# Kernel optimization log

Hardware: AMD Instinct MI355X
Metric: run time of the kernel (lower is better)

Reference implementation:

```python
import jax, jax.numpy as jnp
import numpy as np

E = 1024
H = 16          # num_heads
D = E // H      # head_dim
HID = 1024      # hidden_dim
B, S = 16, 512
EPS = 1e-5


def _ln(x, g, b):
    mu = jnp.mean(x, axis=-1, keepdims=True)
    var = jnp.mean(jnp.square(x - mu), axis=-1, keepdims=True)
    return (x - mu) * jax.lax.rsqrt(var + EPS) * g + b


def setup_inputs() -> dict:
    key = jax.random.key(0)
    ks = jax.random.split(key, 8)
    s = 1.0 / np.sqrt(E)
    return {
        'state_features': jax.random.normal(ks[0], (6, B, S, E), jnp.float32),
        'Wq': jax.random.normal(ks[1], (E, E), jnp.float32) * s,
        'bq': jnp.zeros((E,), jnp.float32),
        'Wk': jax.random.normal(ks[2], (E, E), jnp.float32) * s,
        'bk': jnp.zeros((E,), jnp.float32),
        'Wv': jax.random.normal(ks[3], (E, E), jnp.float32) * s,
        'bv': jnp.zeros((E,), jnp.float32),
        'Wo': jax.random.normal(ks[4], (E, E), jnp.float32) * s,
        'bo': jnp.zeros((E,), jnp.float32),
        'ln1_g': jnp.ones((E,), jnp.float32),
        'ln1_b': jnp.zeros((E,), jnp.float32),
        'fusion_w': jnp.ones((6,), jnp.float32) / 6.0,
        'Wf': jax.random.normal(ks[5], (HID, E), jnp.float32) * s,
        'bf': jnp.zeros((HID,), jnp.float32),
        'ln2_g': jnp.ones((HID,), jnp.float32),
        'ln2_b': jnp.zeros((HID,), jnp.float32),
    }


def reference(state_features, Wq, bq, Wk, bk, Wv, bv, Wo, bo,
              ln1_g, ln1_b, fusion_w, Wf, bf, ln2_g, ln2_b):
    # state_features: (6, B, S, E) -> stacked (N, 6, E), N = B*S
    st = jnp.transpose(state_features, (1, 2, 0, 3)).reshape(B * S, 6, E)
    N = st.shape[0]

    q = (st @ Wq.T + bq).reshape(N, 6, H, D)
    k = (st @ Wk.T + bk).reshape(N, 6, H, D)
    v = (st @ Wv.T + bv).reshape(N, 6, H, D)

    # tiny 6x6 attention per token per head (dropout = identity in eval)
    scores = jnp.einsum('nqhd,nkhd->nhqk', q, k) / np.sqrt(D).astype(np.float32)
    attn = jax.nn.softmax(scores, axis=-1)
    ctx = jnp.einsum('nhqk,nkhd->nqhd', attn, v).reshape(N, 6, E)

    out = ctx @ Wo.T + bo
    enhanced = _ln(out + st, ln1_g, ln1_b)  # (N, 6, E)

    # weighted_sum fusion
    w = jax.nn.softmax(fusion_w)
    fused = jnp.einsum('nse,s->ne', enhanced, w)

    hidden = fused @ Wf.T + bf
    hidden = jnp.where(hidden >= 0, hidden, 0.01 * hidden)  # LeakyReLU(0.01)
    hidden = _ln(hidden, ln2_g, ln2_b)
    return hidden.reshape(B, S, HID)
```

## Files before the change

kernel.cpp:

```cpp
#include <hip/hip_runtime.h>
#include <hip/hip_bf16.h>

#define NTOK 8192
#define E 1024
#define NS 6
#define MBIG (NTOK * NS)
#define NSE ((long)NTOK * E)

typedef short short8 __attribute__((ext_vector_type(8)));
typedef float f32x4 __attribute__((ext_vector_type(4)));
typedef unsigned short ushort4v __attribute__((ext_vector_type(4)));

#define TM 128
#define TN 128
#define BK 64

static __device__ __forceinline__ float bf2f(unsigned short u) {
    union { unsigned int i; float f; } c; c.i = ((unsigned int)u) << 16; return c.f;
}

struct WPtrs { const float* s[5]; __hip_bfloat16* d[5]; };
__global__ __launch_bounds__(256) void cvt5_w(WPtrs p)
{
    const int seg = blockIdx.x >> 10;
    const int i = ((blockIdx.x & 1023) * 256 + threadIdx.x) * 4;
    const float4 v = *(const float4*)(p.s[seg] + i);
    union { __hip_bfloat16 h[4]; unsigned long long u; } pk;
    pk.h[0] = (__hip_bfloat16)v.x;
    pk.h[1] = (__hip_bfloat16)v.y;
    pk.h[2] = (__hip_bfloat16)v.z;
    pk.h[3] = (__hip_bfloat16)v.w;
    *(unsigned long long*)(p.d[seg] + i) = pk.u;
}

__global__ __launch_bounds__(256) void cvt_bulk(
    const float* __restrict__ src, __hip_bfloat16* __restrict__ dst)
{
    const long i = ((long)blockIdx.x * 256 + threadIdx.x) * 4;
    const float4 v = *(const float4*)(src + i);
    union { __hip_bfloat16 h[4]; unsigned long long u; } pk;
    pk.h[0] = (__hip_bfloat16)v.x;
    pk.h[1] = (__hip_bfloat16)v.y;
    pk.h[2] = (__hip_bfloat16)v.z;
    pk.h[3] = (__hip_bfloat16)v.w;
    *(unsigned long long*)(dst + i) = pk.u;
}

#define NITER  8

struct GOut { __hip_bfloat16* C[3]; const float* bias[3]; };

static __device__ __forceinline__ void stage_half(
    const __hip_bfloat16* gsrc,
    __hip_bfloat16* ldst, int tid)
{
#pragma unroll
    for (int piece = 0; piece < 2; ++piece) {
        const int r  = piece * 64 + (tid >> 3);
        const int s  = tid & 7;
        const int ss = s ^ (r & 7);
        const __hip_bfloat16* g = gsrc + (long)r * 1024 + ss * 8;
        __hip_bfloat16* l = ldst + r * 64 + s * 8;
        __builtin_amdgcn_global_load_lds((const __attribute__((address_space(1))) void*)g,
                                         (__attribute__((address_space(3))) void*)l, 16, 0, 0);
    }
}

static __device__ __forceinline__ short8 ld_frag(
    const __hip_bfloat16* half_base, int lr, int slot)
{
    return *(const short8*)(half_base + lr * 64 + ((slot ^ (lr & 7)) << 3));
}

#define STAGE(kt, part)                                                         \
  {                                                                             \
    const int _b  = (kt) & 1;                                                   \
    const int _ab = (part) >> 1;                                                \
    const int _hf = (part) & 1;                                                 \
    const __hip_bfloat16* _g = (_ab == 0)                                       \
        ? A  + (m0 + _hf * 128) * 1024 + (kt) * 64                              \
        : Wb + ((long)n0 + _hf * 128) * 1024 + (kt) * 64;                       \
    stage_half(_g, &lds[((_b * 2 + _ab) * 2 + _hf) * 8192], tid);               \
  }

#define PH(kt, q, HASNEXT, nkt, STMT_STAGE, STMT_WAIT)                          \
  {                                                                             \
    STMT_STAGE;                                                                 \
    STMT_WAIT;                                                                  \
    __builtin_amdgcn_s_barrier();                                               \
    asm volatile("s_waitcnt lgkmcnt(0)" ::: "memory");                          \
    __builtin_amdgcn_sched_barrier(0);                                          \
    __builtin_amdgcn_s_setprio(1);                                              \
    _Pragma("unroll") for (int mf = 0; mf < 2; ++mf)                            \
      _Pragma("unroll") for (int nf = 0; nf < 4; ++nf)                          \
        _Pragma("unroll") for (int k2 = 0; k2 < 2; ++k2)                        \
          acc[(q) * 2 + mf][nf] = __builtin_amdgcn_mfma_f32_16x16x32_bf16(      \
              bfr[nf][k2], afr[(q) & 1][mf][k2], acc[(q) * 2 + mf][nf], 0,0,0); \
    __builtin_amdgcn_s_setprio(0);                                              \
    if ((q) < 3) {                                                              \
      const __hip_bfloat16* _Ab = &lds[((((kt) & 1) * 2 + 0) * 2 + wm) * 8192]; \
      _Pragma("unroll") for (int mf = 0; mf < 2; ++mf)                          \
        _Pragma("unroll") for (int k2 = 0; k2 < 2; ++k2)                        \
          afr[((q) + 1) & 1][mf][k2] =                                          \
              ld_frag(_Ab, ((q) + 1) * 32 + mf * 16 + mrow, k2 * 4 + quad);     \
    } else if (HASNEXT) {                                                       \
      const __hip_bfloat16* _An = &lds[((((nkt) & 1) * 2 + 0) * 2 + wm) * 8192];\
      const __hip_bfloat16* _Bn =                                               \
          &lds[((((nkt) & 1) * 2 + 1) * 2 + (wn >> 1)) * 8192];                 \
      _Pragma("unroll") for (int nf = 0; nf < 4; ++nf)                          \
        _Pragma("unroll") for (int k2 = 0; k2 < 2; ++k2)                        \
          bfr[nf][k2] = ld_frag(_Bn, (wn & 1) * 64 + nf * 16 + mrow,            \
                                k2 * 4 + quad);                                 \
      _Pragma("unroll") for (int mf = 0; mf < 2; ++mf)                          \
        _Pragma("unroll") for (int k2 = 0; k2 < 2; ++k2)                        \
          afr[0][mf][k2] = ld_frag(_An, mf * 16 + mrow, k2 * 4 + quad);         \
    }                                                                           \
    __builtin_amdgcn_s_barrier();                                               \
  }

__global__ __launch_bounds__(512) void gemm256(
    const __hip_bfloat16* __restrict__ A,
    const __hip_bfloat16* __restrict__ Wb,
    GOut out)
{
    __shared__ __hip_bfloat16 lds[2 * 2 * 2 * 8192] __attribute__((aligned(16)));

    const int tid  = threadIdx.x;
    const int lane = tid & 63;
    const int wid  = tid >> 6;
    const int quad = lane >> 4;
    const int mrow = lane & 15;
    const int wm = wid >> 2;
    const int wn = wid & 3;

    const int gx  = gridDim.x;
    const int nwg = gx * gridDim.y;
    const int cpx = nwg >> 3;
    const int lin = blockIdx.y * gx + blockIdx.x;
    const int tile = (lin & 7) * cpx + (lin >> 3);
    const int  n0 = (tile % gx) * 256;
    const long m0 = (long)(tile / gx) * 256;

    f32x4 acc[8][4] = {};
    short8 bfr[4][2];
    short8 afr[2][2][2];

    STAGE(0, 0); STAGE(0, 1); STAGE(0, 2); STAGE(0, 3);
    STAGE(1, 2); STAGE(1, 3);
    asm volatile("s_waitcnt vmcnt(4)" ::: "memory");
    __builtin_amdgcn_s_barrier();

    {
        const __hip_bfloat16* _Ab = &lds[(0 * 2 + wm) * 8192];
        const __hip_bfloat16* _Bb = &lds[((0 * 2 + 1) * 2 + (wn >> 1)) * 8192];
#pragma unroll
        for (int nf = 0; nf < 4; ++nf)
#pragma unroll
            for (int k2 = 0; k2 < 2; ++k2)
                bfr[nf][k2] = ld_frag(_Bb, (wn & 1) * 64 + nf * 16 + mrow, k2 * 4 + quad);
#pragma unroll
        for (int mf = 0; mf < 2; ++mf)
#pragma unroll
            for (int k2 = 0; k2 < 2; ++k2)
                afr[0][mf][k2] = ld_frag(_Ab, mf * 16 + mrow, k2 * 4 + quad);
    }

#pragma unroll 1
    for (int it = 0; it < NITER; ++it) {
        const int kt0 = 2 * it;
        const int kt1 = 2 * it + 1;
        const bool more = (it < NITER - 1);

        PH(kt0, 0, true, kt0, STAGE(kt1, 0), ((void)0));
        PH(kt0, 1, true, kt0, STAGE(kt1, 1), ((void)0));
        PH(kt0, 2, true, kt0, if (more) STAGE(kt0 + 2, 2), ((void)0));
        PH(kt0, 3, true, kt1, if (more) STAGE(kt0 + 2, 3),
           if (more) { asm volatile("s_waitcnt vmcnt(4)" ::: "memory"); }
           else      { asm volatile("s_waitcnt vmcnt(0)" ::: "memory"); });
        PH(kt1, 0, true, kt1, if (more) STAGE(kt0 + 2, 0), ((void)0));
        PH(kt1, 1, true, kt1, if (more) STAGE(kt0 + 2, 1), ((void)0));
        PH(kt1, 2, true, kt1, if (more) STAGE(kt0 + 3, 2), ((void)0));
        PH(kt1, 3, more, kt0 + 2, if (more) STAGE(kt0 + 3, 3),
           if (more) { asm volatile("s_waitcnt vmcnt(4)" ::: "memory"); });
    }

    const int seg = n0 >> 10;
    const int nb  = n0 & 1023;
    __hip_bfloat16* Cp = out.C[seg];
    const float* bp = out.bias[seg];
#pragma unroll
    for (int mf = 0; mf < 8; ++mf) {
        const long row = m0 + wm * 128 + mf * 16 + mrow;
#pragma unroll
        for (int nf = 0; nf < 4; ++nf) {
            const int colb = nb + wn * 64 + nf * 16 + quad * 4;
            const f32x4 bv4 = *(const f32x4*)(bp + colb);
            union { __hip_bfloat16 h[4]; unsigned long long u; } pk;
#pragma unroll
            for (int r = 0; r < 4; ++r)
                pk.h[r] = (__hip_bfloat16)(acc[mf][nf][r] + bv4[r]);
            *(unsigned long long*)(Cp + row * 1024 + colb) = pk.u;
        }
    }
}

__global__ __launch_bounds__(256) void gemm_bt(
    const __hip_bfloat16* __restrict__ A,
    const __hip_bfloat16* __restrict__ Wb,
    const float* __restrict__ bias,
    __hip_bfloat16* __restrict__ C)
{
    __shared__ __hip_bfloat16 lA[TM * BK] __attribute__((aligned(16)));
    __shared__ __hip_bfloat16 lB[TN * BK] __attribute__((aligned(16)));

    const int tid  = threadIdx.x;
    const int wave = tid >> 6;
    const int lane = tid & 63;
    const int quad = lane >> 4;
    const int mrow = lane & 15;
    const int wr = wave >> 1;
    const int wc = wave & 1;

    const int Gy   = gridDim.y;
    const int lin  = blockIdx.y * 8 + blockIdx.x;
    const int tile = (lin & 7) * Gy + (lin >> 3);
    const int  n0 = (tile & 7) * TN;
    const long m0 = (long)(tile >> 3) * TM;

    const int srow = lane >> 3;
    const int scol = (lane & 7) * 8;

    f32x4 acc[4][4] = {};

    for (int k0 = 0; k0 < 1024; k0 += BK) {
        __syncthreads();
#pragma unroll
        for (int it = 0; it < 4; ++it) {
            const int chunk = it * 4 + wave;
            const int row   = chunk * 8 + srow;
            const __hip_bfloat16* ga = A + (m0 + row) * 1024 + k0 + scol;
            const __hip_bfloat16* gb = Wb + (long)(n0 + row) * 1024 + k0 + scol;
            __hip_bfloat16* la = lA + row * BK + scol;
            __hip_bfloat16* lb = lB + row * BK + scol;
            __builtin_amdgcn_global_load_lds((const __attribute__((address_space(1))) void*)ga,
                                             (__attribute__((address_space(3))) void*)la, 16, 0, 0);
            __builtin_amdgcn_global_load_lds((const __attribute__((address_space(1))) void*)gb,
                                             (__attribute__((address_space(3))) void*)lb, 16, 0, 0);
        }
        __syncthreads();

#pragma unroll
        for (int kk = 0; kk < BK; kk += 32) {
            short8 af[4], bfrg[4];
#pragma unroll
            for (int i = 0; i < 4; ++i)
                af[i] = *(const short8*)(lA + (wr * 64 + i * 16 + mrow) * BK + kk + quad * 8);
#pragma unroll
            for (int j = 0; j < 4; ++j)
                bfrg[j] = *(const short8*)(lB + (wc * 64 + j * 16 + mrow) * BK + kk + quad * 8);
#pragma unroll
            for (int i = 0; i < 4; ++i)
#pragma unroll
                for (int j = 0; j < 4; ++j)
                    acc[i][j] = __builtin_amdgcn_mfma_f32_16x16x32_bf16(af[i], bfrg[j], acc[i][j], 0, 0, 0);
        }
    }

#pragma unroll
    for (int i = 0; i < 4; ++i) {
#pragma unroll
        for (int j = 0; j < 4; ++j) {
            const int col = n0 + wc * 64 + j * 16 + mrow;
            const float bv = bias[col];
#pragma unroll
            for (int r = 0; r < 4; ++r) {
                const long row = m0 + wr * 64 + i * 16 + quad * 4 + r;
                C[row * 1024 + col] = (__hip_bfloat16)(acc[i][j][r] + bv);
            }
        }
    }
}

__global__ __launch_bounds__(256) void gemm_a32_bt(
    const float* __restrict__ A,
    const __hip_bfloat16* __restrict__ Wb,
    const float* __restrict__ bias,
    __hip_bfloat16* __restrict__ C)
{
    __shared__ __hip_bfloat16 lA[TM * BK] __attribute__((aligned(16)));
    __shared__ __hip_bfloat16 lB[TN * BK] __attribute__((aligned(16)));

    const int tid  = threadIdx.x;
    const int wave = tid >> 6;
    const int lane = tid & 63;
    const int quad = lane >> 4;
    const int mrow = lane & 15;
    const int wr = wave >> 1;
    const int wc = wave & 1;

    const int Gy   = gridDim.y;
    const int lin  = blockIdx.y * 8 + blockIdx.x;
    const int tile = (lin & 7) * Gy + (lin >> 3);
    const int  n0 = (tile & 7) * TN;
    const long m0 = (long)(tile >> 3) * TM;

    const int srow = lane >> 3;
    const int scol = (lane & 7) * 8;

    f32x4 acc[4][4] = {};

    for (int k0 = 0; k0 < 1024; k0 += BK) {
        __syncthreads();
#pragma unroll
        for (int it = 0; it < 4; ++it) {
            const int chunk = it * 4 + wave;
            const int row   = chunk * 8 + srow;
            const __hip_bfloat16* gb = Wb + (long)(n0 + row) * 1024 + k0 + scol;
            __hip_bfloat16* lb = lB + row * BK + scol;
            __builtin_amdgcn_global_load_lds((const __attribute__((address_space(1))) void*)gb,
                                             (__attribute__((address_space(3))) void*)lb, 16, 0, 0);
        }
#pragma unroll
        for (int u = 0; u < 8; ++u) {
            const int c   = u * 256 + tid;
            const int row = c >> 4;
            const int c4  = c & 15;
            const float4 av = *(const float4*)(A + (m0 + row) * 1024 + k0 + c4 * 4);
            union { __hip_bfloat16 h[4]; unsigned long long uu; } pk;
            pk.h[0] = (__hip_bfloat16)av.x;
            pk.h[1] = (__hip_bfloat16)av.y;
            pk.h[2] = (__hip_bfloat16)av.z;
            pk.h[3] = (__hip_bfloat16)av.w;
            *(unsigned long long*)(lA + row * BK + c4 * 4) = pk.uu;
        }
        __syncthreads();

#pragma unroll
        for (int kk = 0; kk < BK; kk += 32) {
            short8 af[4], bfrg[4];
#pragma unroll
            for (int i = 0; i < 4; ++i)
                af[i] = *(const short8*)(lA + (wr * 64 + i * 16 + mrow) * BK + kk + quad * 8);
#pragma unroll
            for (int j = 0; j < 4; ++j)
                bfrg[j] = *(const short8*)(lB + (wc * 64 + j * 16 + mrow) * BK + kk + quad * 8);
#pragma unroll
            for (int i = 0; i < 4; ++i)
#pragma unroll
                for (int j = 0; j < 4; ++j)
                    acc[i][j] = __builtin_amdgcn_mfma_f32_16x16x32_bf16(af[i], bfrg[j], acc[i][j], 0, 0, 0);
        }
    }

#pragma unroll
    for (int i = 0; i < 4; ++i) {
#pragma unroll
        for (int j = 0; j < 4; ++j) {
            const int col = n0 + wc * 64 + j * 16 + mrow;
            const float bv = bias[col];
#pragma unroll
            for (int r = 0; r < 4; ++r) {
                const long row = m0 + wr * 64 + i * 16 + quad * 4 + r;
                C[row * 1024 + col] = (__hip_bfloat16)(acc[i][j][r] + bv);
            }
        }
    }
}

__global__ __launch_bounds__(256) void attn6(
    const __hip_bfloat16* qb,
    const __hip_bfloat16* __restrict__ kb,
    const __hip_bfloat16* __restrict__ vb,
    __hip_bfloat16* ctx)
{
    const int w    = blockIdx.x * 4 + (threadIdx.x >> 6);
    const int lane = threadIdx.x & 63;
    const int n  = w >> 2;
    const int hg = w & 3;
    const int h  = hg * 4 + (lane >> 4);
    const int sub = lane & 15;
    const long base = (long)n * 1024 + h * 64 + sub * 4;

    float qf[NS][4], kf[NS][4], vf[NS][4];
#pragma unroll
    for (int s = 0; s < NS; ++s) {
        const ushort4v qs = *(const ushort4v*)(qb + s * NSE + base);
        const ushort4v ks = *(const ushort4v*)(kb + s * NSE + base);
        const ushort4v vs = *(const ushort4v*)(vb + s * NSE + base);
#pragma unroll
        for (int c = 0; c < 4; ++c) {
            qf[s][c] = bf2f(qs[c]);
            kf[s][c] = bf2f(ks[c]);
            vf[s][c] = bf2f(vs[c]);
        }
    }

    float p[NS][NS];
#pragma unroll
    for (int i = 0; i < NS; ++i)
#pragma unroll
        for (int j = 0; j < NS; ++j) {
            float t = qf[i][0] * kf[j][0];
            t = fmaf(qf[i][1], kf[j][1], t);
            t = fmaf(qf[i][2], kf[j][2], t);
            t = fmaf(qf[i][3], kf[j][3], t);
            t += __shfl_xor(t, 1, 64);
            t += __shfl_xor(t, 2, 64);
            t += __shfl_xor(t, 4, 64);
            t += __shfl_xor(t, 8, 64);
            p[i][j] = t * 0.125f;
        }

#pragma unroll
    for (int i = 0; i < NS; ++i) {
        float m = p[i][0];
#pragma unroll
        for (int j = 1; j < NS; ++j) m = fmaxf(m, p[i][j]);
        float sum = 0.f;
#pragma unroll
        for (int j = 0; j < NS; ++j) { p[i][j] = __expf(p[i][j] - m); sum += p[i][j]; }
        const float inv = 1.0f / sum;
        float a[4] = {0.f, 0.f, 0.f, 0.f};
#pragma unroll
        for (int j = 0; j < NS; ++j)
#pragma unroll
            for (int c = 0; c < 4; ++c) a[c] = fmaf(p[i][j], vf[j][c], a[c]);
        union { __hip_bfloat16 h4[4]; unsigned long long u; } pk;
#pragma unroll
        for (int c = 0; c < 4; ++c) pk.h4[c] = (__hip_bfloat16)(a[c] * inv);
        *(unsigned long long*)(ctx + i * NSE + base) = pk.u;
    }
}

__global__ __launch_bounds__(256) void ln1_fuse_bf(
    const __hip_bfloat16* __restrict__ wo_out,
    const __hip_bfloat16* __restrict__ sfb,
    const float* __restrict__ g,
    const float* __restrict__ b,
    const float* __restrict__ fw,
    __hip_bfloat16* __restrict__ fused)
{
    const int n = blockIdx.x, tid = threadIdx.x;
    const int wave = tid >> 6, lane = tid & 63;
    const int e0 = tid * 4;

    float w[NS];
    float mx = -1e30f;
#pragma unroll
    for (int s = 0; s < NS; ++s) { w[s] = fw[s]; mx = fmaxf(mx, w[s]); }
    float sw = 0.f;
#pragma unroll
    for (int s = 0; s < NS; ++s) { w[s] = __expf(w[s] - mx); sw += w[s]; }
    const float isw = 1.0f / sw;

    const f32x4 gv4 = *(const f32x4*)(g + e0);
    const f32x4 bv4 = *(const f32x4*)(b + e0);

    __shared__ float red[2][4];
    float accf[4] = {0.f, 0.f, 0.f, 0.f};

    for (int s = 0; s < NS; ++s) {
        const long base = s * NSE + (long)n * 1024 + e0;
        const ushort4v wv = *(const ushort4v*)(wo_out + base);
        const ushort4v sv = *(const ushort4v*)(sfb + base);
        float x[4];
        float sum = 0.f, sq = 0.f;
#pragma unroll
        for (int c = 0; c < 4; ++c) {
            x[c] = bf2f(wv[c]) + bf2f(sv[c]);
            sum += x[c];
            sq  += x[c] * x[c];
        }
#pragma unroll
        for (int off = 32; off; off >>= 1) {
            sum += __shfl_xor(sum, off, 64);
            sq  += __shfl_xor(sq,  off, 64);
        }
        if (lane == 0) { red[0][wave] = sum; red[1][wave] = sq; }
        __syncthreads();
        sum = red[0][0] + red[0][1] + red[0][2] + red[0][3];
        sq  = red[1][0] + red[1][1] + red[1][2] + red[1][3];
        __syncthreads();
        const float mu   = sum * (1.0f / 1024.0f);
        const float var  = sq * (1.0f / 1024.0f) - mu * mu;
        const float rstd = rsqrtf(var + 1e-5f);
        const float ws_  = w[s] * isw;
#pragma unroll
        for (int c = 0; c < 4; ++c)
            accf[c] += ws_ * ((x[c] - mu) * rstd * gv4[c] + bv4[c]);
    }
    union { __hip_bfloat16 h4[4]; unsigned long long u; } pk;
#pragma unroll
    for (int c = 0; c < 4; ++c) pk.h4[c] = (__hip_bfloat16)accf[c];
    *(unsigned long long*)(fused + (long)n * 1024 + e0) = pk.u;
}

__global__ __launch_bounds__(256) void ln1_fuse(
    const __hip_bfloat16* __restrict__ wo_out,
    const float* __restrict__ sf,
    const float* __restrict__ g,
    const float* __restrict__ b,
    const float* __restrict__ fw,
    __hip_bfloat16* __restrict__ fused)
{
    const int n = blockIdx.x, tid = threadIdx.x;
    const int wave = tid >> 6, lane = tid & 63;
    const int e0 = tid * 4;

    float w[NS];
    float mx = -1e30f;
#pragma unroll
    for (int s = 0; s < NS; ++s) { w[s] = fw[s]; mx = fmaxf(mx, w[s]); }
    float sw = 0.f;
#pragma unroll
    for (int s = 0; s < NS; ++s) { w[s] = __expf(w[s] - mx); sw += w[s]; }
    const float isw = 1.0f / sw;

    const f32x4 gv4 = *(const f32x4*)(g + e0);
    const f32x4 bv4 = *(const f32x4*)(b + e0);

    __shared__ float red[2][4];
    float accf[4] = {0.f, 0.f, 0.f, 0.f};

    for (int s = 0; s < NS; ++s) {
        const long base = s * NSE + (long)n * 1024 + e0;
        const ushort4v wv = *(const ushort4v*)(wo_out + base);
        const f32x4   sv = *(const f32x4*)(sf + base);
        float x[4];
        float sum = 0.f, sq = 0.f;
#pragma unroll
        for (int c = 0; c < 4; ++c) {
            x[c] = bf2f(wv[c]) + sv[c];
            sum += x[c];
            sq  += x[c] * x[c];
        }
#pragma unroll
        for (int off = 32; off; off >>= 1) {
            sum += __shfl_xor(sum, off, 64);
            sq  += __shfl_xor(sq,  off, 64);
        }
        if (lane == 0) { red[0][wave] = sum; red[1][wave] = sq; }
        __syncthreads();
        sum = red[0][0] + red[0][1] + red[0][2] + red[0][3];
        sq  = red[1][0] + red[1][1] + red[1][2] + red[1][3];
        __syncthreads();
        const float mu   = sum * (1.0f / 1024.0f);
        const float var  = sq * (1.0f / 1024.0f) - mu * mu;
        const float rstd = rsqrtf(var + 1e-5f);
        const float ws_  = w[s] * isw;
#pragma unroll
        for (int c = 0; c < 4; ++c)
            accf[c] += ws_ * ((x[c] - mu) * rstd * gv4[c] + bv4[c]);
    }
    union { __hip_bfloat16 h4[4]; unsigned long long u; } pk;
#pragma unroll
    for (int c = 0; c < 4; ++c) pk.h4[c] = (__hip_bfloat16)accf[c];
    *(unsigned long long*)(fused + (long)n * 1024 + e0) = pk.u;
}

__global__ __launch_bounds__(256) void ln2_out(
    const __hip_bfloat16* __restrict__ hidden,
    const float* __restrict__ g,
    const float* __restrict__ b,
    float* __restrict__ out)
{
    const int n = blockIdx.x, tid = threadIdx.x;
    const int wave = tid >> 6, lane = tid & 63;
    const int e0 = tid * 4;
    __shared__ float red[2][4];

    const ushort4v hv = *(const ushort4v*)(hidden + (long)n * 1024 + e0);
    float x[4];
    float sum = 0.f, sq = 0.f;
#pragma unroll
    for (int c = 0; c < 4; ++c) {
        float t = bf2f(hv[c]);
        t = t >= 0.f ? t : 0.01f * t;
        x[c] = t;
        sum += t;
        sq  += t * t;
    }
#pragma unroll
    for (int off = 32; off; off >>= 1) {
        sum += __shfl_xor(sum, off, 64);
        sq  += __shfl_xor(sq,  off, 64);
    }
    if (lane == 0) { red[0][wave] = sum; red[1][wave] = sq; }
    __syncthreads();
    sum = red[0][0] + red[0][1] + red[0][2] + red[0][3];
    sq  = red[1][0] + red[1][1] + red[1][2] + red[1][3];
    const float mu   = sum * (1.0f / 1024.0f);
    const float var  = sq * (1.0f / 1024.0f) - mu * mu;
    const float rstd = rsqrtf(var + 1e-5f);

    const f32x4 gv4 = *(const f32x4*)(g + e0);
    const f32x4 bv4 = *(const f32x4*)(b + e0);
    f32x4 o;
#pragma unroll
    for (int c = 0; c < 4; ++c)
        o[c] = (x[c] - mu) * rstd * gv4[c] + bv4[c];
    *(f32x4*)(out + (long)n * 1024 + e0) = o;
}

extern "C" void kernel_launch(void* const* d_in, const int* in_sizes, int n_in,
                              void* d_out, int out_size, void* d_ws, size_t ws_size,
                              hipStream_t stream)
{
    const float* SF  = (const float*)d_in[0];
    const float* Wq  = (const float*)d_in[1];
    const float* bq  = (const float*)d_in[2];
    const float* Wk  = (const float*)d_in[3];
    const float* bk  = (const float*)d_in[4];
    const float* Wv  = (const float*)d_in[5];
    const float* bv  = (const float*)d_in[6];
    const float* Wo  = (const float*)d_in[7];
    const float* bo  = (const float*)d_in[8];
    const float* g1  = (const float*)d_in[9];
    const float* b1  = (const float*)d_in[10];
    const float* fw  = (const float*)d_in[11];
    const float* Wf  = (const float*)d_in[12];
    const float* bf_ = (const float*)d_in[13];
    const float* g2  = (const float*)d_in[14];
    const float* b2  = (const float*)d_in[15];
    float* out = (float*)d_out;

    const size_t REG = (size_t)MBIG * 1024 * sizeof(__hip_bfloat16);
    const size_t WTS = (size_t)5 * 1024 * 1024 * sizeof(__hip_bfloat16);
    const bool big_ws = ws_size >= 4 * REG + WTS;

    __hip_bfloat16* r0  = (__hip_bfloat16*)d_ws;
    __hip_bfloat16* r1  = r0 + (long)MBIG * 1024;
    __hip_bfloat16* r2  = r1 + (long)MBIG * 1024;
    __hip_bfloat16* r3  = r2 + (long)MBIG * 1024;
    __hip_bfloat16* wb  = big_ws ? (r3 + (long)MBIG * 1024) : r3;
    __hip_bfloat16* Wqb = wb;
    __hip_bfloat16* Wkb = Wqb + 1024 * 1024;
    __hip_bfloat16* Wvb = Wkb + 1024 * 1024;
    __hip_bfloat16* Wob = Wvb + 1024 * 1024;
    __hip_bfloat16* Wfb = Wob + 1024 * 1024;

    const dim3 blk(256);

    WPtrs wp;
    wp.s[0] = Wq; wp.s[1] = Wk; wp.s[2] = Wv; wp.s[3] = Wo; wp.s[4] = Wf;
    wp.d[0] = Wqb; wp.d[1] = Wkb; wp.d[2] = Wvb; wp.d[3] = Wob; wp.d[4] = Wfb;
    cvt5_w<<<5 * 1024, blk, 0, stream>>>(wp);

    cvt_bulk<<<MBIG, blk, 0, stream>>>(SF, r2);

    if (big_ws) {
        const dim3 blk2(512);
        const dim3 gQKV(12, MBIG / 256);
        const dim3 gB2(4, MBIG / 256);

        GOut oqkv;
        oqkv.C[0] = r0; oqkv.C[1] = r1; oqkv.C[2] = r3;
        oqkv.bias[0] = bq; oqkv.bias[1] = bk; oqkv.bias[2] = bv;
        gemm256<<<gQKV, blk2, 0, stream>>>(r2, Wqb, oqkv);

        attn6<<<NTOK, blk, 0, stream>>>(r0, r1, r3, r0);

        GOut owo;
        owo.C[0] = r1; owo.C[1] = r1; owo.C[2] = r1;
        owo.bias[0] = bo; owo.bias[1] = bo; owo.bias[2] = bo;
        gemm256<<<gB2, blk2, 0, stream>>>(r0, Wob, owo);

        ln1_fuse_bf<<<NTOK, blk, 0, stream>>>(r1, r2, g1, b1, fw, r0);

        gemm_bt<<<dim3(8, NTOK / TM), blk, 0, stream>>>(r0, Wfb, bf_, r2);

        ln2_out<<<NTOK, blk, 0, stream>>>(r2, g2, b2, out);
    } else {
        const dim3 gBig(8, MBIG / TM);
        const dim3 gSm(8, NTOK / TM);

        gemm_bt<<<gBig, blk, 0, stream>>>(r2, Wqb, bq, r0);
        gemm_bt<<<gBig, blk, 0, stream>>>(r2, Wkb, bk, r1);
        gemm_a32_bt<<<gBig, blk, 0, stream>>>(SF, Wvb, bv, r2);
        attn6<<<NTOK, blk, 0, stream>>>(r0, r1, r2, r0);
        gemm_bt<<<gBig, blk, 0, stream>>>(r0, Wob, bo, r1);
        ln1_fuse<<<NTOK, blk, 0, stream>>>(r1, SF, g1, b1, fw, r2);
        gemm_bt<<<gSm, blk, 0, stream>>>(r2, Wfb, bf_, r0);
        ln2_out<<<NTOK, blk, 0, stream>>>(r0, g2, b2, out);
    }
}
```

Before: 921.4 us.

## Fuse residual add into Wo GEMM epilogue and use wave-per-row layernorm kernels

The Wo GEMM epilogue now adds the bf16 residual (converted state features) directly, so the layernorm-fusion kernel reads one bf16 tensor per slot instead of two. The LN1-fusion and LN2 kernels are rewritten so that one wavefront handles a whole 1024-wide row with 16 elements per lane. This removes the shared-memory reductions and block barriers in favour of pure wave shuffles. The residual is now rounded to bf16 together with the GEMM output before layernorm, which adds a little rounding error.

```diff
diff --git a/kernel.cpp b/kernel.cpp
--- a/kernel.cpp
+++ b/kernel.cpp
@@ -10,6 +10,7 @@
 typedef short short8 __attribute__((ext_vector_type(8)));
 typedef float f32x4 __attribute__((ext_vector_type(4)));
 typedef unsigned short ushort4v __attribute__((ext_vector_type(4)));
+typedef unsigned short ushort8v __attribute__((ext_vector_type(8)));
 
 #define TM 128
 #define TN 128
@@ -48,7 +49,7 @@
 
 #define NITER  8
 
-struct GOut { __hip_bfloat16* C[3]; const float* bias[3]; };
+struct GOut { __hip_bfloat16* C[3]; const float* bias[3]; const __hip_bfloat16* R; };
 
 static __device__ __forceinline__ void stage_half(
     const __hip_bfloat16* gsrc,
@@ -188,6 +189,7 @@
     const int nb  = n0 & 1023;
     __hip_bfloat16* Cp = out.C[seg];
     const float* bp = out.bias[seg];
+    const bool hasR = (out.R != nullptr);
 #pragma unroll
     for (int mf = 0; mf < 8; ++mf) {
         const long row = m0 + wm * 128 + mf * 16 + mrow;
@@ -195,10 +197,16 @@
         for (int nf = 0; nf < 4; ++nf) {
             const int colb = nb + wn * 64 + nf * 16 + quad * 4;
             const f32x4 bv4 = *(const f32x4*)(bp + colb);
+            float rs[4] = {0.f, 0.f, 0.f, 0.f};
+            if (hasR) {
+                const ushort4v rv = *(const ushort4v*)(out.R + row * 1024 + colb);
+#pragma unroll
+                for (int r = 0; r < 4; ++r) rs[r] = bf2f(rv[r]);
+            }
             union { __hip_bfloat16 h[4]; unsigned long long u; } pk;
 #pragma unroll
             for (int r = 0; r < 4; ++r)
-                pk.h[r] = (__hip_bfloat16)(acc[mf][nf][r] + bv4[r]);
+                pk.h[r] = (__hip_bfloat16)(acc[mf][nf][r] + bv4[r] + rs[r]);
             *(unsigned long long*)(Cp + row * 1024 + colb) = pk.u;
         }
     }
@@ -432,14 +440,80 @@
     }
 }
 
-__global__ __launch_bounds__(256) void ln1_fuse_bf(
-    const __hip_bfloat16* __restrict__ wo_out,
-    const __hip_bfloat16* __restrict__ sfb,
+__global__ __launch_bounds__(256) void ln1_fuse_w(
+    const __hip_bfloat16* __restrict__ enh,
     const float* __restrict__ g,
     const float* __restrict__ b,
     const float* __restrict__ fw,
     __hip_bfloat16* __restrict__ fused)
 {
+    const int wave = threadIdx.x >> 6, lane = threadIdx.x & 63;
+    const int n  = blockIdx.x * 4 + wave;
+    const int e0 = lane * 16;
+
+    float w[NS];
+    float mx = -1e30f;
+#pragma unroll
+    for (int s = 0; s < NS; ++s) { w[s] = fw[s]; mx = fmaxf(mx, w[s]); }
+    float sw = 0.f;
+#pragma unroll
+    for (int s = 0; s < NS; ++s) { w[s] = __expf(w[s] - mx); sw += w[s]; }
+    const float isw = 1.0f / sw;
+
+    f32x4 gq[4], bq4[4];
+#pragma unroll
+    for (int c4 = 0; c4 < 4; ++c4) {
+        gq[c4]  = *(const f32x4*)(g + e0 + c4 * 4);
+        bq4[c4] = *(const f32x4*)(b + e0 + c4 * 4);
+    }
+
+    float accf[16];
+#pragma unroll
+    for (int c = 0; c < 16; ++c) accf[c] = 0.f;
+
+#pragma unroll
+    for (int s = 0; s < NS; ++s) {
+        const long base = s * NSE + (long)n * 1024 + e0;
+        const ushort8v h0 = *(const ushort8v*)(enh + base);
+        const ushort8v h1 = *(const ushort8v*)(enh + base + 8);
+        float x[16];
+#pragma unroll
+        for (int c = 0; c < 8; ++c) { x[c] = bf2f(h0[c]); x[8 + c] = bf2f(h1[c]); }
+        float sum = 0.f, sq = 0.f;
+#pragma unroll
+        for (int c = 0; c < 16; ++c) { sum += x[c]; sq += x[c] * x[c]; }
+#pragma unroll
+        for (int off = 32; off; off >>= 1) {
+            sum += __shfl_xor(sum, off, 64);
+            sq  += __shfl_xor(sq,  off, 64);
+        }
+        const float mu   = sum * (1.0f / 1024.0f);
+        const float var  = sq * (1.0f / 1024.0f) - mu * mu;
+        const float rstd = rsqrtf(var + 1e-5f);
+        const float ws_  = w[s] * isw;
+#pragma unroll
+        for (int c4 = 0; c4 < 4; ++c4)
+#pragma unroll
+            for (int j = 0; j < 4; ++j)
+                accf[c4 * 4 + j] += ws_ * ((x[c4 * 4 + j] - mu) * rstd * gq[c4][j] + bq4[c4][j]);
+    }
+#pragma unroll
+    for (int c4 = 0; c4 < 4; ++c4) {
+        union { __hip_bfloat16 h4[4]; unsigned long long u; } pk;
+#pragma unroll
+        for (int j = 0; j < 4; ++j) pk.h4[j] = (__hip_bfloat16)accf[c4 * 4 + j];
+        *(unsigned long long*)(fused + (long)n * 1024 + e0 + c4 * 4) = pk.u;
+    }
+}
+
+__global__ __launch_bounds__(256) void ln1_fuse(
+    const __hip_bfloat16* __restrict__ wo_out,
+    const float* __restrict__ sf,
+    const float* __restrict__ g,
+    const float* __restrict__ b,
+    const float* __restrict__ fw,
+    __hip_bfloat16* __restrict__ fused)
+{
     const int n = blockIdx.x, tid = threadIdx.x;
     const int wave = tid >> 6, lane = tid & 63;
     const int e0 = tid * 4;
@@ -462,12 +536,12 @@
     for (int s = 0; s < NS; ++s) {
         const long base = s * NSE + (long)n * 1024 + e0;
         const ushort4v wv = *(const ushort4v*)(wo_out + base);
-        const ushort4v sv = *(const ushort4v*)(sfb + base);
+        const f32x4   sv = *(const f32x4*)(sf + base);
         float x[4];
         float sum = 0.f, sq = 0.f;
 #pragma unroll
         for (int c = 0; c < 4; ++c) {
-            x[c] = bf2f(wv[c]) + bf2f(sv[c]);
+            x[c] = bf2f(wv[c]) + sv[c];
             sum += x[c];
             sq  += x[c] * x[c];
         }
@@ -495,67 +569,47 @@
     *(unsigned long long*)(fused + (long)n * 1024 + e0) = pk.u;
 }
 
-__global__ __launch_bounds__(256) void ln1_fuse(
-    const __hip_bfloat16* __restrict__ wo_out,
-    const float* __restrict__ sf,
+__global__ __launch_bounds__(256) void ln2_out_w(
+    const __hip_bfloat16* __restrict__ hidden,
     const float* __restrict__ g,
     const float* __restrict__ b,
-    const float* __restrict__ fw,
-    __hip_bfloat16* __restrict__ fused)
-{
-    const int n = blockIdx.x, tid = threadIdx.x;
-    const int wave = tid >> 6, lane = tid & 63;
-    const int e0 = tid * 4;
-
-    float w[NS];
-    float mx = -1e30f;
-#pragma unroll
-    for (int s = 0; s < NS; ++s) { w[s] = fw[s]; mx = fmaxf(mx, w[s]); }
-    float sw = 0.f;
-#pragma unroll
-    for (int s = 0; s < NS; ++s) { w[s] = __expf(w[s] - mx); sw += w[s]; }
-    const float isw = 1.0f / sw;
-
-    const f32x4 gv4 = *(const f32x4*)(g + e0);
-    const f32x4 bv4 = *(const f32x4*)(b + e0);
-
-    __shared__ float red[2][4];
-    float accf[4] = {0.f, 0.f, 0.f, 0.f};
-
-    for (int s = 0; s < NS; ++s) {
-        const long base = s * NSE + (long)n * 1024 + e0;
-        const ushort4v wv = *(const ushort4v*)(wo_out + base);
-        const f32x4   sv = *(const f32x4*)(sf + base);
-        float x[4];
-        float sum = 0.f, sq = 0.f;
-#pragma unroll
-        for (int c = 0; c < 4; ++c) {
-            x[c] = bf2f(wv[c]) + sv[c];
-            sum += x[c];
-            sq  += x[c] * x[c];
-        }
-#pragma unroll
-        for (int off = 32; off; off >>= 1) {
-            sum += __shfl_xor(sum, off, 64);
-            sq  += __shfl_xor(sq,  off, 64);
-        }
-        if (lane == 0) { red[0][wave] = sum; red[1][wave] = sq; }
-        __syncthreads();
-        sum = red[0][0] + red[0][1] + red[0][2] + red[0][3];
-        sq  = red[1][0] + red[1][1] + red[1][2] + red[1][3];
-        __syncthreads();
-        const float mu   = sum * (1.0f / 1024.0f);
-        const float var  = sq * (1.0f / 1024.0f) - mu * mu;
-        const float rstd = rsqrtf(var + 1e-5f);
-        const float ws_  = w[s] * isw;
-#pragma unroll
-        for (int c = 0; c < 4; ++c)
-            accf[c] += ws_ * ((x[c] - mu) * rstd * gv4[c] + bv4[c]);
-    }
-    union { __hip_bfloat16 h4[4]; unsigned long long u; } pk;
-#pragma unroll
-    for (int c = 0; c < 4; ++c) pk.h4[c] = (__hip_bfloat16)accf[c];
-    *(unsigned long long*)(fused + (long)n * 1024 + e0) = pk.u;
+    float* __restrict__ out)
+{
+    const int wave = threadIdx.x >> 6, lane = threadIdx.x & 63;
+    const int n  = blockIdx.x * 4 + wave;
+    const int e0 = lane * 16;
+
+    const ushort8v h0 = *(const ushort8v*)(hidden + (long)n * 1024 + e0);
+    const ushort8v h1 = *(const ushort8v*)(hidden + (long)n * 1024 + e0 + 8);
+    float x[16];
+    float sum = 0.f, sq = 0.f;
+#pragma unroll
+    for (int c = 0; c < 8; ++c) {
+        float t0 = bf2f(h0[c]); t0 = t0 >= 0.f ? t0 : 0.01f * t0;
+        float t1 = bf2f(h1[c]); t1 = t1 >= 0.f ? t1 : 0.01f * t1;
+        x[c] = t0; x[8 + c] = t1;
+    }
+#pragma unroll
+    for (int c = 0; c < 16; ++c) { sum += x[c]; sq += x[c] * x[c]; }
+#pragma unroll
+    for (int off = 32; off; off >>= 1) {
+        sum += __shfl_xor(sum, off, 64);
+        sq  += __shfl_xor(sq,  off, 64);
+    }
+    const float mu   = sum * (1.0f / 1024.0f);
+    const float var  = sq * (1.0f / 1024.0f) - mu * mu;
+    const float rstd = rsqrtf(var + 1e-5f);
+
+#pragma unroll
+    for (int c4 = 0; c4 < 4; ++c4) {
+        const f32x4 gv4 = *(const f32x4*)(g + e0 + c4 * 4);
+        const f32x4 bv4 = *(const f32x4*)(b + e0 + c4 * 4);
+        f32x4 o;
+#pragma unroll
+        for (int j = 0; j < 4; ++j)
+            o[j] = (x[c4 * 4 + j] - mu) * rstd * gv4[j] + bv4[j];
+        *(f32x4*)(out + (long)n * 1024 + e0 + c4 * 4) = o;
+    }
 }
 
 __global__ __launch_bounds__(256) void ln2_out(
@@ -656,6 +710,7 @@
         GOut oqkv;
         oqkv.C[0] = r0; oqkv.C[1] = r1; oqkv.C[2] = r3;
         oqkv.bias[0] = bq; oqkv.bias[1] = bk; oqkv.bias[2] = bv;
+        oqkv.R = nullptr;
         gemm256<<<gQKV, blk2, 0, stream>>>(r2, Wqb, oqkv);
 
         attn6<<<NTOK, blk, 0, stream>>>(r0, r1, r3, r0);
@@ -663,13 +718,14 @@
         GOut owo;
         owo.C[0] = r1; owo.C[1] = r1; owo.C[2] = r1;
         owo.bias[0] = bo; owo.bias[1] = bo; owo.bias[2] = bo;
+        owo.R = r2;
         gemm256<<<gB2, blk2, 0, stream>>>(r0, Wob, owo);
 
-        ln1_fuse_bf<<<NTOK, blk, 0, stream>>>(r1, r2, g1, b1, fw, r0);
+        ln1_fuse_w<<<NTOK / 4, blk, 0, stream>>>(r1, g1, b1, fw, r0);
 
         gemm_bt<<<dim3(8, NTOK / TM), blk, 0, stream>>>(r0, Wfb, bf_, r2);
 
-        ln2_out<<<NTOK, blk, 0, stream>>>(r2, g2, b2, out);
+        ln2_out_w<<<NTOK / 4, blk, 0, stream>>>(r2, g2, b2, out);
     } else {
         const dim3 gBig(8, MBIG / TM);
         const dim3 gSm(8, NTOK / TM);
```

After: 924.8 us. No clear change (+0.4%).
